# Optimization experiments

Measured on AMD Instinct MI355X. Metric: run time of the kernel, lower is better.

Reference implementation:

```python
import jax, jax.numpy as jnp
import numpy as np

N = 50000; E = 800000; IN = 128; OUT = 64; ED = 16; H = 4
NEG_SLOPE = 0.2


def adaptive_avg_pool1d(v, L):
    """torch F.adaptive_avg_pool1d on a 1-D vector v -> length L (static slices)."""
    S = v.shape[0]
    return jnp.stack([v[(i * S) // L: -((-(i + 1) * S) // L)].mean() for i in range(L)])


def gat_conv(x, edge_index, edge_attr, W_gat, att_src, att_dst, W_edge, att_edge, b_gat):
    """PyG GATConv(heads=H, concat=False, edge_dim=ED), eval mode (no dropout)."""
    n = x.shape[0]
    h, c = att_src.shape
    xs = (x @ W_gat).reshape(n, h, c)                       # [N,H,C]
    a_src = jnp.einsum('nhc,hc->nh', xs, att_src)           # [N,H]
    a_dst = jnp.einsum('nhc,hc->nh', xs, att_dst)           # [N,H]
    e = (edge_attr @ W_edge).reshape(-1, h, c)              # [E,H,C]
    a_edge = jnp.einsum('ehc,hc->eh', e, att_edge)          # [E,H]
    src, dst = edge_index[0], edge_index[1]
    alpha = a_src[src] + a_dst[dst] + a_edge                # [E,H]
    alpha = jax.nn.leaky_relu(alpha, NEG_SLOPE)
    # segment softmax over incoming edges of each destination node
    amax = jax.ops.segment_max(alpha, dst, num_segments=n)  # [N,H]
    ex = jnp.exp(alpha - amax[dst])
    denom = jax.ops.segment_sum(ex, dst, num_segments=n)
    alpha = ex / (denom[dst] + 1e-16)
    msg = xs[src] * alpha[:, :, None]                       # [E,H,C]
    out = jax.ops.segment_sum(msg, dst, num_segments=n)     # [N,H,C]
    return out.mean(axis=1) + b_gat                         # concat=False -> head mean


def setup_inputs():
    key = jax.random.key(0)
    ks = jax.random.split(key, 16)
    p = lambda k, s: jax.random.normal(k, s, dtype=jnp.float32) * 0.05
    return {
        'x': jax.random.normal(ks[0], (N, IN), dtype=jnp.float32),
        'edge_index': jax.random.randint(ks[1], (2, E), 0, N),
        'edge_attr': jax.random.normal(ks[2], (E, ED), dtype=jnp.float32),
        'quality_raw': jax.random.uniform(ks[3], (E, 4), dtype=jnp.float32),
        'network_state': jax.random.uniform(ks[4], (8,), dtype=jnp.float32),
        'W_gat': p(ks[5], (IN, H * OUT)),
        'att_src': p(ks[6], (H, OUT)),
        'att_dst': p(ks[7], (H, OUT)),
        'W_edge': p(ks[8], (ED, H * OUT)),
        'att_edge': p(ks[9], (H, OUT)),
        'b_gat': jnp.zeros((OUT,), jnp.float32),
        'W_q1': p(ks[10], (4, ED // 2)),
        'b_q1': jnp.zeros((ED // 2,), jnp.float32),
        'W_q2': p(ks[11], (ED // 2, ED)),
        'b_q2': jnp.zeros((ED,), jnp.float32),
        'W_c': p(ks[12], (OUT + ED, OUT)),
        'b_c': jnp.zeros((OUT,), jnp.float32),
    }


def reference(x, edge_index, edge_attr, quality_raw, network_state,
              W_gat, att_src, att_dst, W_edge, att_edge, b_gat,
              W_q1, b_q1, W_q2, b_q2, W_c, b_c):
    # vectorized path-quality encoder (replaces per-edge python loop)
    q = jax.nn.relu(quality_raw @ W_q1 + b_q1) @ W_q2 + b_q2      # [E,ED]
    enhanced_edge_attr = edge_attr + q
    x_conv = gat_conv(x, edge_index, enhanced_edge_attr,
                      W_gat, att_src, att_dst, W_edge, att_edge, b_gat)  # [N,OUT]
    cf = adaptive_avg_pool1d(network_state, ED)                    # [ED]
    cf = jnp.broadcast_to(cf, (x.shape[0], ED))                    # [N,ED]
    h = jnp.concatenate([x_conv, cf], axis=-1)                     # [N,OUT+ED]
    return jax.nn.relu(h @ W_c + b_c)                              # [N,OUT]
```

## Files before the change

kernel.cpp:

```cpp
#include <hip/hip_runtime.h>
#include <hip/hip_bf16.h>

#define NN 50000
#define EE 800000
#define NEG 0.2f
#define NSH 8
#define NS (NN*NSH)
#define NSB2 98
#define NZB 98
#define NGB 1563
#define NDB 782

using u32 = unsigned int;
typedef short short4v __attribute__((ext_vector_type(4)));
typedef float f32x4 __attribute__((ext_vector_type(4)));
typedef unsigned int u32x4 __attribute__((ext_vector_type(4)));

__device__ __forceinline__ unsigned short f2bf(float f){
  u32 b = __float_as_uint(f);
  b += 0x7FFFu + ((b >> 16) & 1u);
  return (unsigned short)(b >> 16);
}

__global__ __launch_bounds__(256) void k_pre_all(
        const float* __restrict__ Wg, const float* __restrict__ W_c,
        const float* __restrict__ W_edge, const float* __restrict__ att_edge,
        const float* __restrict__ b_c, const float* __restrict__ ns,
        const float* __restrict__ b_gat,
        const float* __restrict__ att_src, const float* __restrict__ att_dst,
        unsigned short* __restrict__ WzB, float* __restrict__ Wt,
        float* __restrict__ cvec, uint2* __restrict__ avp,
        u32* __restrict__ deg8){
  int bid = blockIdx.x, tid = threadIdx.x;
  if (bid < 128){
    __shared__ float sWg[256];
    __shared__ float sWc[64*64];
    sWg[tid] = Wg[bid*256 + tid];
    for (int i = tid; i < 4096; i += 256) sWc[i] = W_c[i];
    __syncthreads();
    int h = tid >> 6, j = tid & 63;
    float s = 0.f;
    #pragma unroll 8
    for (int c = 0; c < 64; c++) s += sWg[h*64 + c] * sWc[c*64 + j];
    int t = tid >> 4, lr = tid & 15;
    int ks = bid >> 4, lg = (bid >> 2) & 3, q = bid & 3;
    int l = lg*16 + lr;
    WzB[(((t*8 + ks)*64 + l) << 2) + q] = f2bf(s);
  } else if (bid == 128){
    if (tid < 64){
      int d = tid >> 2, h = tid & 3;
      float s = 0.f;
      for (int c = 0; c < 64; c++) s += W_edge[d*256 + h*64 + c] * att_edge[h*64 + c];
      Wt[d*4 + h] = s;
    } else if (tid < 128){
      int j = tid - 64;
      float s = b_c[j];
      for (int d = 0; d < 16; d++) s += ns[d >> 1] * W_c[(64 + d)*64 + j];
      for (int c = 0; c < 64; c++) s += b_gat[c] * W_c[c*64 + j];
      cvec[j] = s;
    }
  } else if (bid == 129){
    __shared__ float sav2[1024];
    for (int i = tid; i < 1024; i += 256){
      int k = i >> 3, o = i & 7, h = o & 3;
      const float* att = (o < 4) ? att_src : att_dst;
      float s = 0.f;
      for (int c = 0; c < 64; c++) s += Wg[k*256 + h*64 + c] * att[h*64 + c];
      sav2[i] = s;
    }
    __syncthreads();
    if (tid < 64){
      int l = tid, lg = l >> 4, lr = l & 15;
      for (int ks = 0; ks < 8; ks++){
        unsigned int h0, h1, h2, h3;
        int kb = ks*16 + lg*4;
        h0 = (lr < 8) ? f2bf(sav2[(kb+0)*8 + lr]) : 0u;
        h1 = (lr < 8) ? f2bf(sav2[(kb+1)*8 + lr]) : 0u;
        h2 = (lr < 8) ? f2bf(sav2[(kb+2)*8 + lr]) : 0u;
        h3 = (lr < 8) ? f2bf(sav2[(kb+3)*8 + lr]) : 0u;
        uint2 u; u.x = h0 | (h1 << 16); u.y = h2 | (h3 << 16);
        avp[ks*64 + l] = u;
      }
    }
  } else {
    u32x4 z = {0u,0u,0u,0u};
    int slot0 = ((bid - 130)*256 + tid)*4;
    #pragma unroll
    for (int i = 0; i < 4; i++){
      int slot = slot0 + i;
      if (slot*4 < NS) *(u32x4*)(deg8 + slot*4) = z;
    }
  }
}

__global__ __launch_bounds__(256) void k_main(const float* __restrict__ x,
        const unsigned short* __restrict__ WzB, const uint2* __restrict__ avp,
        const int* __restrict__ dsts,
        __hip_bfloat16* __restrict__ zs,
        float* __restrict__ a_src, float* __restrict__ a_dst,
        u32* __restrict__ deg8, unsigned short* __restrict__ rank){
  __shared__ alignas(16) char ldsu[17408];
  int tid = threadIdx.x;
  int bid = blockIdx.x;

  if ((bid % 3) == 1){
    int g = bid / 3;
    int gi = g*256 + tid;
    if (gi*4 < EE){
      int shard = g & (NSH-1);
      int4 d4 = *(const int4*)(dsts + (size_t)gi*4);
      u32 r0 = atomicAdd(&deg8[((size_t)(u32)d4.x << 3) | shard], 1u);
      u32 r1 = atomicAdd(&deg8[((size_t)(u32)d4.y << 3) | shard], 1u);
      u32 r2 = atomicAdd(&deg8[((size_t)(u32)d4.z << 3) | shard], 1u);
      u32 r3 = atomicAdd(&deg8[((size_t)(u32)d4.w << 3) | shard], 1u);
      uint2 pk;
      pk.x = (r0 & 0xffffu) | (r1 << 16);
      pk.y = (r2 & 0xffffu) | (r3 << 16);
      *(uint2*)(rank + (size_t)gi*4) = pk;
    }
    return;
  }

  int gb = bid - (bid + 2)/3;
  int w = tid >> 6, l = tid & 63;
  int lr = l & 15, lg = l >> 4;
  int rw = w >> 1, ch = w & 1;
  int nb = gb*32;
  int n0 = nb + rw*16;

  float* xsl = (float*)ldsu;
  __hip_bfloat16* ztp = (__hip_bfloat16*)ldsu;

  {
    float4 stg[4];
    #pragma unroll
    for (int i = 0; i < 4; i++){
      int s = w*256 + i*64 + l;
      int r = s >> 5, c = s & 31;
      int row = nb + r; if (row >= NN) row = NN - 1;
      stg[i] = *(const float4*)(x + (size_t)row*128 + c*4);
    }
    #pragma unroll
    for (int i = 0; i < 4; i++){
      int s = w*256 + i*64 + l;
      *(float4*)(xsl + s*4) = stg[i];
    }
  }
  __syncthreads();

  short4v afr[8];
  #pragma unroll
  for (int ks = 0; ks < 8; ks++){
    float4 xa = *(const float4*)(xsl + ((rw*16 + lr)*128 + ks*16 + lg*4));
    short4v a;
    a[0] = (short)f2bf(xa.x); a[1] = (short)f2bf(xa.y);
    a[2] = (short)f2bf(xa.z); a[3] = (short)f2bf(xa.w);
    afr[ks] = a;
  }
  if (ch == 0){
    f32x4 cad = {0.f, 0.f, 0.f, 0.f};
    #pragma unroll
    for (int ks = 0; ks < 8; ks++){
      short4v b = __builtin_bit_cast(short4v, avp[ks*64 + l]);
      cad = __builtin_amdgcn_mfma_f32_16x16x16bf16_1k(afr[ks], b, cad, 0, 0, 0);
    }
    #pragma unroll
    for (int r = 0; r < 4; r++){
      int n = n0 + lg*4 + r;
      if (n < NN){
        if (lr < 4)      a_src[(size_t)n*4 + lr]       = cad[r];
        else if (lr < 8) a_dst[(size_t)n*4 + (lr - 4)] = cad[r];
      }
    }
  }
  __syncthreads();

  #pragma unroll 4
  for (int t8 = 0; t8 < 8; t8++){
    int t = ch*8 + t8;
    f32x4 c = {0.f, 0.f, 0.f, 0.f};
    #pragma unroll
    for (int ks = 0; ks < 8; ks++){
      short4v b = *(const short4v*)(WzB + (((t*8 + ks)*64 + l) << 2));
      c = __builtin_amdgcn_mfma_f32_16x16x16bf16_1k(afr[ks], b, c, 0, 0, 0);
    }
    #pragma unroll
    for (int r = 0; r < 4; r++)
      ztp[((w*16) + lg*4 + r)*136 + t8*16 + lr] = __float2bfloat16(c[r]);
  }
  #pragma unroll
  for (int i = 0; i < 4; i++){
    int f = i*64 + l;
    int row = f >> 4, c16 = f & 15;
    int n = n0 + row;
    if (n < NN)
      *(uint4*)(zs + (size_t)n*256 + ch*128 + c16*8) = *(const uint4*)&ztp[(w*16 + row)*136 + c16*8];
  }
}

__global__ __launch_bounds__(1024) void k_scan1(const u32* __restrict__ deg8,
                                                u32* __restrict__ offs8, u32* __restrict__ bsum){
  __shared__ u32 sd[1024];
  int t = threadIdx.x;
  size_t base = (size_t)blockIdx.x*4096 + (size_t)t*4;
  u32x4 v = {0u,0u,0u,0u};
  if (base < NS) v = *(const u32x4*)(deg8 + base);
  u32 o1 = v.x, o2 = o1 + v.y, o3 = o2 + v.z;
  u32 tsum = o3 + v.w;
  sd[t] = tsum; __syncthreads();
  for (int off = 1; off < 1024; off <<= 1){
    u32 u = (t >= off) ? sd[t-off] : 0u;
    __syncthreads();
    sd[t] += u;
    __syncthreads();
  }
  u32 excl = sd[t] - tsum;
  if (base < NS){
    u32x4 o = {excl, excl + o1, excl + o2, excl + o3};
    *(u32x4*)(offs8 + base) = o;
  }
  if (t == 1023) bsum[blockIdx.x] = sd[1023];
}

__global__ __launch_bounds__(1024) void k_scan2(u32* __restrict__ offs8,
                                                const u32* __restrict__ bsum){
  __shared__ u32 sd[1024];
  int b = blockIdx.x, t = threadIdx.x;
  sd[t] = (t < b) ? bsum[t] : 0u;
  __syncthreads();
  #pragma unroll
  for (int off = 512; off; off >>= 1){
    if (t < off) sd[t] += sd[t + off];
    __syncthreads();
  }
  u32 p = sd[0];
  size_t base = (size_t)b*4096 + (size_t)t*4;
  if (base < NS){
    u32x4 o = *(u32x4*)(offs8 + base);
    o.x += p; o.y += p; o.z += p; o.w += p;
    *(u32x4*)(offs8 + base) = o;
  }
  if (b == 0 && t == 0) offs8[NS] = EE;
}

__global__ __launch_bounds__(256) void k_edge(const float* __restrict__ qraw,
        const float* __restrict__ eattr, const int* __restrict__ eidx,
        const float* __restrict__ Wq1, const float* __restrict__ bq1,
        const float* __restrict__ Wq2, const float* __restrict__ bq2,
        const float* __restrict__ Wt,
        const float* __restrict__ a_src,
        const u32* __restrict__ offs8, const unsigned short* __restrict__ rank,
        uint4* __restrict__ csr){
  __shared__ float sWq1[32], sbq1[8], sWq2[128], sbq2[16], sWt[64];
  int tid = threadIdx.x;
  if (tid < 32) sWq1[tid] = Wq1[tid];
  else if (tid < 40)  sbq1[tid-32]  = bq1[tid-32];
  else if (tid < 168) sWq2[tid-40]  = Wq2[tid-40];
  else if (tid < 184) sbq2[tid-168] = bq2[tid-168];
  else if (tid < 248) sWt[tid-184]  = Wt[tid-184];
  __syncthreads();
  int e = blockIdx.x*256 + tid;
  if (e >= EE) return;
  int shard = (blockIdx.x >> 2) & (NSH-1);

  int src = eidx[e], dst = eidx[EE + e];
  u32 rk = (u32)rank[e];
  float4 qr = *(const float4*)(qraw + (size_t)e*4);
  float4 as4 = *(const float4*)(a_src + (size_t)src*4);
  u32 base = offs8[((size_t)(u32)dst << 3) | shard];

  float t1[8];
  #pragma unroll
  for (int j = 0; j < 8; j++){
    float s = sbq1[j] + qr.x*sWq1[j] + qr.y*sWq1[8+j] + qr.z*sWq1[16+j] + qr.w*sWq1[24+j];
    t1[j] = fmaxf(s, 0.f);
  }
  float ae[4] = {0.f,0.f,0.f,0.f};
  const float* ea = eattr + (size_t)e*16;
  #pragma unroll
  for (int d = 0; d < 16; d++){
    float q = sbq2[d];
    #pragma unroll
    for (int j = 0; j < 8; j++) q += t1[j]*sWq2[j*16 + d];
    float v = ea[d] + q;
    #pragma unroll
    for (int h = 0; h < 4; h++) ae[h] += v * sWt[d*4 + h];
  }
  u32 pk0 = (u32)f2bf(as4.x + ae[0]);
  u32 pk1 = (u32)f2bf(as4.y + ae[1]);
  u32 pk2 = (u32)f2bf(as4.z + ae[2]);
  u32 pk3 = (u32)f2bf(as4.w + ae[3]);
  u32 pos = base + rk;
  uint4 q;
  q.x = (u32)src;
  q.y = pk0 | (pk1 << 16);
  q.z = pk2 | (pk3 << 16);
  q.w = 0u;
  csr[pos] = q;
}

__global__ __launch_bounds__(256) void k_agg(const __hip_bfloat16* __restrict__ zs,
        const uint4* __restrict__ csr, const u32* __restrict__ offs8,
        const float* __restrict__ a_dst,
        const float* __restrict__ cvec, float* __restrict__ out){
  int tid = threadIdx.x;
  int w = tid >> 6, lane = tid & 63;
  int half = lane >> 5, sl = lane & 31;
  int n = blockIdx.x*8 + w*2 + half;
  int h = sl >> 3, c8 = sl & 7;
  u32 p0 = offs8[(size_t)n << 3], p1 = offs8[((size_t)n << 3) + 8];
  float adv = a_dst[((size_t)n << 2) + h];
  int sh = (h & 1) ? 0 : 16;
  u32 lb = (u32)(h*128 + c8*16);
  const char* zb = (const char*)zs;
  float d = 0.f;
  float a0=0.f,a1=0.f,a2=0.f,a3=0.f,a4=0.f,a5=0.f,a6=0.f,a7=0.f;
  u32 p = p0;
  for (; p + 4 <= p1; p += 4){
    uint4 q0 = csr[p+0], q1 = csr[p+1], q2 = csr[p+2], q3 = csr[p+3];
    u32 s0 = q0.x, s1 = q1.x, s2 = q2.x, s3 = q3.x;
    u32 w0p = (h < 2) ? q0.y : q0.z,  w1p = (h < 2) ? q1.y : q1.z;
    u32 w2p = (h < 2) ? q2.y : q2.z,  w3p = (h < 2) ? q3.y : q3.z;
    uint4 v0 = *(const uint4*)(zb + ((s0 << 9) + lb));
    uint4 v1 = *(const uint4*)(zb + ((s1 << 9) + lb));
    uint4 v2 = *(const uint4*)(zb + ((s2 << 9) + lb));
    uint4 v3 = *(const uint4*)(zb + ((s3 << 9) + lb));
    float al0 = __uint_as_float((w0p << sh) & 0xffff0000u) + adv;
    float al1 = __uint_as_float((w1p << sh) & 0xffff0000u) + adv;
    float al2 = __uint_as_float((w2p << sh) & 0xffff0000u) + adv;
    float al3 = __uint_as_float((w3p << sh) & 0xffff0000u) + adv;
    al0 = fmaxf(al0, 0.f) + NEG*fminf(al0, 0.f);
    al1 = fmaxf(al1, 0.f) + NEG*fminf(al1, 0.f);
    al2 = fmaxf(al2, 0.f) + NEG*fminf(al2, 0.f);
    al3 = fmaxf(al3, 0.f) + NEG*fminf(al3, 0.f);
    float w0 = __expf(al0), w1 = __expf(al1), w2 = __expf(al2), w3 = __expf(al3);
    a0 += w0*__uint_as_float(v0.x << 16)         + w1*__uint_as_float(v1.x << 16)
        + w2*__uint_as_float(v2.x << 16)         + w3*__uint_as_float(v3.x << 16);
    a1 += w0*__uint_as_float(v0.x & 0xffff0000u) + w1*__uint_as_float(v1.x & 0xffff0000u)
        + w2*__uint_as_float(v2.x & 0xffff0000u) + w3*__uint_as_float(v3.x & 0xffff0000u);
    a2 += w0*__uint_as_float(v0.y << 16)         + w1*__uint_as_float(v1.y << 16)
        + w2*__uint_as_float(v2.y << 16)         + w3*__uint_as_float(v3.y << 16);
    a3 += w0*__uint_as_float(v0.y & 0xffff0000u) + w1*__uint_as_float(v1.y & 0xffff0000u)
        + w2*__uint_as_float(v2.y & 0xffff0000u) + w3*__uint_as_float(v3.y & 0xffff0000u);
    a4 += w0*__uint_as_float(v0.z << 16)         + w1*__uint_as_float(v1.z << 16)
        + w2*__uint_as_float(v2.z << 16)         + w3*__uint_as_float(v3.z << 16);
    a5 += w0*__uint_as_float(v0.z & 0xffff0000u) + w1*__uint_as_float(v1.z & 0xffff0000u)
        + w2*__uint_as_float(v2.z & 0xffff0000u) + w3*__uint_as_float(v3.z & 0xffff0000u);
    a6 += w0*__uint_as_float(v0.w << 16)         + w1*__uint_as_float(v1.w << 16)
        + w2*__uint_as_float(v2.w << 16)         + w3*__uint_as_float(v3.w << 16);
    a7 += w0*__uint_as_float(v0.w & 0xffff0000u) + w1*__uint_as_float(v1.w & 0xffff0000u)
        + w2*__uint_as_float(v2.w & 0xffff0000u) + w3*__uint_as_float(v3.w & 0xffff0000u);
    d  += (w0 + w1) + (w2 + w3);
  }
  for (; p < p1; p++){
    uint4 q0 = csr[p];
    u32 wp = (h < 2) ? q0.y : q0.z;
    float al = __uint_as_float((wp << sh) & 0xffff0000u) + adv;
    al = fmaxf(al, 0.f) + NEG*fminf(al, 0.f);
    float w0 = __expf(al);
    uint4 v0 = *(const uint4*)(zb + ((q0.x << 9) + lb));
    a0 += w0*__uint_as_float(v0.x << 16);
    a1 += w0*__uint_as_float(v0.x & 0xffff0000u);
    a2 += w0*__uint_as_float(v0.y << 16);
    a3 += w0*__uint_as_float(v0.y & 0xffff0000u);
    a4 += w0*__uint_as_float(v0.z << 16);
    a5 += w0*__uint_as_float(v0.z & 0xffff0000u);
    a6 += w0*__uint_as_float(v0.w << 16);
    a7 += w0*__uint_as_float(v0.w & 0xffff0000u);
    d  += w0;
  }
  float inv = (d > 0.f) ? 0.25f / d : 0.f;
  a0 *= inv; a1 *= inv; a2 *= inv; a3 *= inv;
  a4 *= inv; a5 *= inv; a6 *= inv; a7 *= inv;
  a0 += __shfl_xor(a0, 8);  a1 += __shfl_xor(a1, 8);
  a2 += __shfl_xor(a2, 8);  a3 += __shfl_xor(a3, 8);
  a4 += __shfl_xor(a4, 8);  a5 += __shfl_xor(a5, 8);
  a6 += __shfl_xor(a6, 8);  a7 += __shfl_xor(a7, 8);
  a0 += __shfl_xor(a0, 16); a1 += __shfl_xor(a1, 16);
  a2 += __shfl_xor(a2, 16); a3 += __shfl_xor(a3, 16);
  a4 += __shfl_xor(a4, 16); a5 += __shfl_xor(a5, 16);
  a6 += __shfl_xor(a6, 16); a7 += __shfl_xor(a7, 16);
  if (h == 0){
    const float* cv = cvec + c8*8;
    float4 o0, o1v;
    o0.x  = fmaxf(a0 + cv[0], 0.f);
    o0.y  = fmaxf(a1 + cv[1], 0.f);
    o0.z  = fmaxf(a2 + cv[2], 0.f);
    o0.w  = fmaxf(a3 + cv[3], 0.f);
    o1v.x = fmaxf(a4 + cv[4], 0.f);
    o1v.y = fmaxf(a5 + cv[5], 0.f);
    o1v.z = fmaxf(a6 + cv[6], 0.f);
    o1v.w = fmaxf(a7 + cv[7], 0.f);
    float* op = out + (size_t)n*64 + c8*8;
    *(float4*)op = o0;
    *(float4*)(op + 4) = o1v;
  }
}

extern "C" void kernel_launch(void* const* d_in, const int* in_sizes, int n_in,
                              void* d_out, int out_size, void* d_ws, size_t ws_size,
                              hipStream_t stream){
  const float* x       = (const float*)d_in[0];
  const int*   eidx    = (const int*)d_in[1];
  const float* eattr   = (const float*)d_in[2];
  const float* qraw    = (const float*)d_in[3];
  const float* ns      = (const float*)d_in[4];
  const float* Wg      = (const float*)d_in[5];
  const float* att_src = (const float*)d_in[6];
  const float* att_dst = (const float*)d_in[7];
  const float* W_edge  = (const float*)d_in[8];
  const float* att_edge= (const float*)d_in[9];
  const float* b_gat   = (const float*)d_in[10];
  const float* Wq1     = (const float*)d_in[11];
  const float* bq1     = (const float*)d_in[12];
  const float* Wq2     = (const float*)d_in[13];
  const float* bq2     = (const float*)d_in[14];
  const float* W_c     = (const float*)d_in[15];
  const float* b_c     = (const float*)d_in[16];
  float* out = (float*)d_out;

  char* ws = (char*)d_ws;
  __hip_bfloat16* zs = (__hip_bfloat16*)ws;
  uint4* csr      = (uint4*)(ws + 25600000);
  u32* deg8       = (u32*)(ws + 25600000);
  u32* offs8      = (u32*)(ws + 38400000);
  float* a_src    = (float*)(ws + 41600064);
  float* a_dst    = (float*)(ws + 42400064);
  unsigned short* rank = (unsigned short*)(ws + 43200064);
  u32* bsum       = (u32*)(ws + 44800064);
  unsigned short* WzB = (unsigned short*)(ws + 44804160);
  uint2* avp      = (uint2*)(ws + 44869696);
  float* Wt       = (float*)(ws + 44873792);
  float* cvec     = (float*)(ws + 44874048);

  k_pre_all<<<130+NZB,  256, 0, stream>>>(Wg, W_c, W_edge, att_edge, b_c, ns, b_gat,
                                          att_src, att_dst, WzB, Wt, cvec, avp, deg8);
  k_main   <<<NGB+NDB,  256, 0, stream>>>(x, WzB, avp, eidx + EE, zs, a_src, a_dst,
                                          deg8, rank);
  k_scan1  <<<NSB2,    1024, 0, stream>>>(deg8, offs8, bsum);
  k_scan2  <<<NSB2,    1024, 0, stream>>>(offs8, bsum);
  k_edge   <<<3125,     256, 0, stream>>>(qraw, eattr, eidx, Wq1, bq1, Wq2, bq2, Wt,
                                          a_src, offs8, rank, csr);
  k_agg    <<<6250,     256, 0, stream>>>(zs, csr, offs8, a_dst, cvec, out);
}
```

Baseline: 159.0 us.

## Move per-edge quality MLP into degree-count blocks of main kernel

The per-edge path-quality MLP and edge attention projection now run inside the degree-counting blocks of k_main. They write a bf16 a_edge buffer to workspace, and a slimmer k_edge_f later combines it with a_src and scatters into the CSR. The aim is to hide the MLP arithmetic and the edge_attr/quality reads behind the atomics-bound phase, taking them off the critical path after the scans. The cost is an extra 6.4MB write and read, a second bf16 rounding of a_edge, and a fallback path when the workspace is too small.

```diff
diff --git a/kernel.cpp b/kernel.cpp
--- a/kernel.cpp
+++ b/kernel.cpp
@@ -96,14 +96,36 @@
 __global__ __launch_bounds__(256) void k_main(const float* __restrict__ x,
         const unsigned short* __restrict__ WzB, const uint2* __restrict__ avp,
         const int* __restrict__ dsts,
+        const float* __restrict__ qraw, const float* __restrict__ eattr,
+        const float* __restrict__ Wq1, const float* __restrict__ bq1,
+        const float* __restrict__ Wq2, const float* __restrict__ bq2,
+        const float* __restrict__ Wt,
         __hip_bfloat16* __restrict__ zs,
         float* __restrict__ a_src, float* __restrict__ a_dst,
-        u32* __restrict__ deg8, unsigned short* __restrict__ rank){
+        u32* __restrict__ deg8, unsigned short* __restrict__ rank,
+        uint2* __restrict__ aeb, int do_mlp){
   __shared__ alignas(16) char ldsu[17408];
   int tid = threadIdx.x;
   int bid = blockIdx.x;
 
   if ((bid % 3) == 1){
+    float* swq = (float*)ldsu;
+    if (tid < 248){
+      float v;
+      if (tid < 32)       v = Wq1[tid];
+      else if (tid < 40)  v = bq1[tid-32];
+      else if (tid < 168) v = Wq2[tid-40];
+      else if (tid < 184) v = bq2[tid-168];
+      else                v = Wt[tid-184];
+      swq[tid] = v;
+    }
+    __syncthreads();
+    const float* sWq1 = swq;
+    const float* sbq1 = swq + 32;
+    const float* sWq2 = swq + 40;
+    const float* sbq2 = swq + 168;
+    const float* sWt  = swq + 184;
+
     int g = bid / 3;
     int gi = g*256 + tid;
     if (gi*4 < EE){
@@ -117,6 +139,35 @@
       pk.x = (r0 & 0xffffu) | (r1 << 16);
       pk.y = (r2 & 0xffffu) | (r3 << 16);
       *(uint2*)(rank + (size_t)gi*4) = pk;
+    }
+    if (do_mlp){
+      #pragma unroll
+      for (int k = 0; k < 4; k++){
+        int e = g*1024 + k*256 + tid;
+        if (e >= EE) break;
+        float4 qr = *(const float4*)(qraw + (size_t)e*4);
+        float t1[8];
+        #pragma unroll
+        for (int j = 0; j < 8; j++){
+          float s = sbq1[j] + qr.x*sWq1[j] + qr.y*sWq1[8+j] + qr.z*sWq1[16+j] + qr.w*sWq1[24+j];
+          t1[j] = fmaxf(s, 0.f);
+        }
+        float ae[4] = {0.f,0.f,0.f,0.f};
+        const float* ea = eattr + (size_t)e*16;
+        #pragma unroll
+        for (int d = 0; d < 16; d++){
+          float q = sbq2[d];
+          #pragma unroll
+          for (int j = 0; j < 8; j++) q += t1[j]*sWq2[j*16 + d];
+          float v = ea[d] + q;
+          #pragma unroll
+          for (int h = 0; h < 4; h++) ae[h] += v * sWt[d*4 + h];
+        }
+        uint2 u;
+        u.x = (u32)f2bf(ae[0]) | ((u32)f2bf(ae[1]) << 16);
+        u.y = (u32)f2bf(ae[2]) | ((u32)f2bf(ae[3]) << 16);
+        aeb[e] = u;
+      }
     }
     return;
   }
@@ -243,7 +294,35 @@
   if (b == 0 && t == 0) offs8[NS] = EE;
 }
 
-__global__ __launch_bounds__(256) void k_edge(const float* __restrict__ qraw,
+__global__ __launch_bounds__(256) void k_edge_f(const int* __restrict__ eidx,
+        const unsigned short* __restrict__ rank, const uint2* __restrict__ aeb,
+        const float* __restrict__ a_src, const u32* __restrict__ offs8,
+        uint4* __restrict__ csr){
+  int e = blockIdx.x*256 + threadIdx.x;
+  if (e >= EE) return;
+  int shard = (blockIdx.x >> 2) & (NSH-1);
+  int src = eidx[e], dst = eidx[EE + e];
+  u32 rk = (u32)rank[e];
+  uint2 ae2 = aeb[e];
+  float4 as4 = *(const float4*)(a_src + (size_t)src*4);
+  u32 base = offs8[((size_t)(u32)dst << 3) | shard];
+  float ae0 = __uint_as_float(ae2.x << 16);
+  float ae1 = __uint_as_float(ae2.x & 0xffff0000u);
+  float ae2v = __uint_as_float(ae2.y << 16);
+  float ae3 = __uint_as_float(ae2.y & 0xffff0000u);
+  u32 pk0 = (u32)f2bf(as4.x + ae0);
+  u32 pk1 = (u32)f2bf(as4.y + ae1);
+  u32 pk2 = (u32)f2bf(as4.z + ae2v);
+  u32 pk3 = (u32)f2bf(as4.w + ae3);
+  uint4 q;
+  q.x = (u32)src;
+  q.y = pk0 | (pk1 << 16);
+  q.z = pk2 | (pk3 << 16);
+  q.w = 0u;
+  csr[base + rk] = q;
+}
+
+__global__ __launch_bounds__(256) void k_edge_s(const float* __restrict__ qraw,
         const float* __restrict__ eattr, const int* __restrict__ eidx,
         const float* __restrict__ Wq1, const float* __restrict__ bq1,
         const float* __restrict__ Wq2, const float* __restrict__ bq2,
@@ -290,13 +369,12 @@
   u32 pk1 = (u32)f2bf(as4.y + ae[1]);
   u32 pk2 = (u32)f2bf(as4.z + ae[2]);
   u32 pk3 = (u32)f2bf(as4.w + ae[3]);
-  u32 pos = base + rk;
   uint4 q;
   q.x = (u32)src;
   q.y = pk0 | (pk1 << 16);
   q.z = pk2 | (pk3 << 16);
   q.w = 0u;
-  csr[pos] = q;
+  csr[base + rk] = q;
 }
 
 __global__ __launch_bounds__(256) void k_agg(const __hip_bfloat16* __restrict__ zs,
@@ -432,14 +510,21 @@
   uint2* avp      = (uint2*)(ws + 44869696);
   float* Wt       = (float*)(ws + 44873792);
   float* cvec     = (float*)(ws + 44874048);
+  uint2* aeb      = (uint2*)(ws + 44874304);
+  int big = (ws_size >= (size_t)44874304 + 6400000) ? 1 : 0;
 
   k_pre_all<<<130+NZB,  256, 0, stream>>>(Wg, W_c, W_edge, att_edge, b_c, ns, b_gat,
                                           att_src, att_dst, WzB, Wt, cvec, avp, deg8);
-  k_main   <<<NGB+NDB,  256, 0, stream>>>(x, WzB, avp, eidx + EE, zs, a_src, a_dst,
-                                          deg8, rank);
+  k_main   <<<NGB+NDB,  256, 0, stream>>>(x, WzB, avp, eidx + EE, qraw, eattr,
+                                          Wq1, bq1, Wq2, bq2, Wt,
+                                          zs, a_src, a_dst, deg8, rank, aeb, big);
   k_scan1  <<<NSB2,    1024, 0, stream>>>(deg8, offs8, bsum);
   k_scan2  <<<NSB2,    1024, 0, stream>>>(offs8, bsum);
-  k_edge   <<<3125,     256, 0, stream>>>(qraw, eattr, eidx, Wq1, bq1, Wq2, bq2, Wt,
+  if (big){
+    k_edge_f<<<3125,    256, 0, stream>>>(eidx, rank, aeb, a_src, offs8, csr);
+  } else {
+    k_edge_s<<<3125,    256, 0, stream>>>(qraw, eattr, eidx, Wq1, bq1, Wq2, bq2, Wt,
                                           a_src, offs8, rank, csr);
+  }
   k_agg    <<<6250,     256, 0, stream>>>(zs, csr, offs8, a_dst, cvec, out);
 }
```

Measured after the change: 155.4 us. 2.2% less time.
